# Kernel tuning notes

Hardware: AMD Instinct MI355X
Metric: run time of the kernel (lower is better)

Reference implementation:

```python
import jax, jax.numpy as jnp
import numpy as np

B, C_IN, C_OUT, K, H, W = 16, 256, 512, 7, 64, 64
PAD = K // 2


def setup_inputs() -> dict:
    key = jax.random.key(0)
    k1, k2, k3 = jax.random.split(key, 3)
    x = jax.random.normal(k1, (B, C_IN, H, W), dtype=jnp.float32)
    # depthwise weight: [out_channels=C_IN, in_channels//groups=1, k, k]
    fan_dw = 1 * K * K
    dw_w = jax.random.normal(k2, (C_IN, 1, K, K), dtype=jnp.float32) * np.sqrt(2.0 / fan_dw)
    dw_b = jnp.zeros((C_IN,), dtype=jnp.float32)
    # pointwise weight: [C_OUT, C_IN, 1, 1]
    pw_w = jax.random.normal(k3, (C_OUT, C_IN, 1, 1), dtype=jnp.float32) * np.sqrt(2.0 / C_IN)
    pw_b = jnp.zeros((C_OUT,), dtype=jnp.float32)
    return {"x": x, "dw_w": dw_w, "dw_b": dw_b, "pw_w": pw_w, "pw_b": pw_b}


def reference(x, dw_w, dw_b, pw_w, pw_b):
    # Depthwise conv (groups == C_in): cross-correlation, same as the torch
    # unfold+einsum construction with zero padding k//2.
    y = jax.lax.conv_general_dilated(
        x, dw_w,
        window_strides=(1, 1),
        padding=[(PAD, PAD), (PAD, PAD)],
        feature_group_count=C_IN,
        dimension_numbers=("NCHW", "OIHW", "NCHW"),
    )
    y = y + dw_b[None, :, None, None]
    # Pointwise 1x1 conv == per-pixel GEMM over channels.
    out = jnp.einsum("bchw,oc->bohw", y, pw_w[:, :, 0, 0])
    out = out + pw_b[None, :, None, None]
    return out
```

## Files before the change

kernel.cpp:

```cpp
#include <hip/hip_runtime.h>

typedef unsigned short US;
typedef __bf16 bf16x8 __attribute__((ext_vector_type(8)));
typedef float f32x4 __attribute__((ext_vector_type(4)));

__device__ __forceinline__ US f2bf(float f) {
  union { float f; unsigned u; } v; v.f = f;
  unsigned r = v.u + 0x7fffu + ((v.u >> 16) & 1u);
  return (US)(r >> 16);
}

__global__ __launch_bounds__(256) void k_convw(const float* __restrict__ pw,
                                               US* __restrict__ wb) {
  int i = (blockIdx.x * 256 + threadIdx.x) * 4;
  float4 v = *(const float4*)(pw + i);
  ushort4 s;
  s.x = f2bf(v.x); s.y = f2bf(v.y); s.z = f2bf(v.z); s.w = f2bf(v.w);
  *(ushort4*)(wb + i) = s;
}

__global__ __launch_bounds__(512, 4) void k_dw(const float* __restrict__ x,
                                               const float* __restrict__ dww,
                                               const float* __restrict__ dwb,
                                               US* __restrict__ y8) {
  const int bid = blockIdx.x;
  const int rg  = bid & 3;
  const int cg  = (bid >> 2) & 31;
  const int b   = bid >> 7;
  const int t   = threadIdx.x;
  const int w   = t >> 6;
  const int l   = t & 63;
  const int g   = l >> 4;
  const int cb  = l & 15;
  const int c   = __builtin_amdgcn_readfirstlane(cg * 8 + w);
  const float* xp = x + ((size_t)b * 256 + c) * 4096;
  float wv[49];
  const float* wp = dww + c * 49;
#pragma unroll
  for (int i = 0; i < 49; ++i) wv[i] = wp[i];
  const float bias = dwb[c];

  const int r0  = rg * 16;
  const int br  = r0 + g * 4;
  const int bcx = cb * 4;

  float acc[4][4];
#pragma unroll
  for (int o = 0; o < 4; ++o)
#pragma unroll
    for (int q = 0; q < 4; ++q) acc[o][q] = bias;

#pragma unroll
  for (int j = 0; j < 10; ++j) {
    const int r = br - 3 + j;
    float L[12];
    if ((unsigned)r < 64u) {
      const float* rp = xp + r * 64 + bcx;
      float4 a = (bcx >= 4) ? *(const float4*)(rp - 4) : float4{0.f, 0.f, 0.f, 0.f};
      float4 bb = *(const float4*)(rp);
      float4 cc = (bcx < 60) ? *(const float4*)(rp + 4) : float4{0.f, 0.f, 0.f, 0.f};
      L[0]=a.x; L[1]=a.y; L[2]=a.z;  L[3]=a.w;
      L[4]=bb.x; L[5]=bb.y; L[6]=bb.z; L[7]=bb.w;
      L[8]=cc.x; L[9]=cc.y; L[10]=cc.z; L[11]=cc.w;
    } else {
#pragma unroll
      for (int i2 = 0; i2 < 12; ++i2) L[i2] = 0.f;
    }
#pragma unroll
    for (int o = 0; o < 4; ++o) {
      if (j - o >= 0 && j - o <= 6) {
        const int kh = j - o;
#pragma unroll
        for (int kw = 0; kw < 7; ++kw) {
          const float wk = wv[kh * 7 + kw];
#pragma unroll
          for (int q = 0; q < 4; ++q)
            acc[o][q] = fmaf(L[q + kw + 1], wk, acc[o][q]);
        }
      }
    }
  }

  __shared__ US t8[8][1024];
#pragma unroll
  for (int o = 0; o < 4; ++o) {
    ushort4 s;
    s.x = f2bf(acc[o][0]); s.y = f2bf(acc[o][1]);
    s.z = f2bf(acc[o][2]); s.w = f2bf(acc[o][3]);
    *(ushort4*)&t8[w][(g * 4 + o) * 64 + bcx] = s;
  }
  __syncthreads();

  unsigned rc[8];
#pragma unroll
  for (int c2 = 0; c2 < 8; ++c2) rc[c2] = *(const unsigned*)&t8[c2][2 * t];
  uint4 A, B2;
  A.x  = __builtin_amdgcn_perm(rc[1], rc[0], 0x05040100u);
  A.y  = __builtin_amdgcn_perm(rc[3], rc[2], 0x05040100u);
  A.z  = __builtin_amdgcn_perm(rc[5], rc[4], 0x05040100u);
  A.w  = __builtin_amdgcn_perm(rc[7], rc[6], 0x05040100u);
  B2.x = __builtin_amdgcn_perm(rc[1], rc[0], 0x07060302u);
  B2.y = __builtin_amdgcn_perm(rc[3], rc[2], 0x07060302u);
  B2.z = __builtin_amdgcn_perm(rc[5], rc[4], 0x07060302u);
  B2.w = __builtin_amdgcn_perm(rc[7], rc[6], 0x07060302u);
  US* yb = y8 + (((size_t)b * 32 + cg) * 4096 + r0 * 64) * 8 + (size_t)t * 16;
  *(uint4*)(yb)     = A;
  *(uint4*)(yb + 8) = B2;
}

__global__ __launch_bounds__(256, 2) void k_pw(const US* __restrict__ y8,
                                               const US* __restrict__ wb,
                                               const float* __restrict__ pwb,
                                               float* __restrict__ out) {
  const int bid = blockIdx.x;
  const int s   = ((bid & 7) << 8) | (bid >> 3);
  const int b   = s >> 7;
  const int rr  = s & 127;
  const int nt  = rr >> 2;
  const int mt  = rr & 3;
  const int o0  = mt * 128;
  const int hw0 = nt * 128;

  __shared__ US lsA[2][128][72];
  __shared__ US lsB[2][128][72];
  const int tid  = threadIdx.x;
  const int lane = tid & 63;
  const int wid  = tid >> 6;
  const int wm   = wid >> 1, wn = wid & 1;
  const int strow = tid >> 3;
  const int scg   = tid & 7;
  const int bg    = tid >> 5;
  const int bl    = tid & 31;

  const f32x4 fzero = {0.f, 0.f, 0.f, 0.f};
  f32x4 acc[4][4];
#pragma unroll
  for (int m = 0; m < 4; ++m)
#pragma unroll
    for (int n = 0; n < 4; ++n) acc[m][n] = fzero;

  uint4 ra[4], rb[4];
#pragma unroll
  for (int i = 0; i < 4; ++i) {
    ra[i] = *(const uint4*)(wb + (size_t)(o0 + i * 32 + strow) * 256 + scg * 8);
    rb[i] = *(const uint4*)(y8 + ((size_t)(b * 32 + bg) * 4096 + hw0 + bl + 32 * i) * 8);
  }
#pragma unroll
  for (int i = 0; i < 4; ++i) {
    *(uint4*)&lsA[0][i * 32 + strow][scg * 8] = ra[i];
    *(uint4*)&lsB[0][bl + 32 * i][bg * 8]     = rb[i];
  }
  __syncthreads();

  for (int kt = 0; kt < 4; ++kt) {
    const int cur = kt & 1;
    if (kt < 3) {
      const int ck = (kt + 1) * 64;
#pragma unroll
      for (int i = 0; i < 4; ++i) {
        ra[i] = *(const uint4*)(wb + (size_t)(o0 + i * 32 + strow) * 256 + ck + scg * 8);
        rb[i] = *(const uint4*)(y8 + ((size_t)(b * 32 + (ck >> 3) + bg) * 4096 + hw0 + bl + 32 * i) * 8);
      }
    }
    bf16x8 af[2][4], bfr[2][4];
#pragma unroll
    for (int kk = 0; kk < 2; ++kk) {
      const int kcol = kk * 32 + (lane >> 4) * 8;
#pragma unroll
      for (int m = 0; m < 4; ++m)
        af[kk][m] = *reinterpret_cast<const bf16x8*>(&lsA[cur][wm * 64 + m * 16 + (lane & 15)][kcol]);
#pragma unroll
      for (int n = 0; n < 4; ++n)
        bfr[kk][n] = *reinterpret_cast<const bf16x8*>(&lsB[cur][wn * 64 + n * 16 + (lane & 15)][kcol]);
    }
#pragma unroll
    for (int kk = 0; kk < 2; ++kk)
#pragma unroll
      for (int m = 0; m < 4; ++m)
#pragma unroll
        for (int n = 0; n < 4; ++n)
          acc[m][n] = __builtin_amdgcn_mfma_f32_16x16x32_bf16(bfr[kk][n], af[kk][m], acc[m][n], 0, 0, 0);

    if (kt < 3) {
#pragma unroll
      for (int i = 0; i < 4; ++i) {
        *(uint4*)&lsA[cur ^ 1][i * 32 + strow][scg * 8] = ra[i];
        *(uint4*)&lsB[cur ^ 1][bl + 32 * i][bg * 8]     = rb[i];
      }
      __syncthreads();
    }
  }

#pragma unroll
  for (int m = 0; m < 4; ++m) {
    const int o  = o0 + wm * 64 + m * 16 + (lane & 15);
    const float bv = pwb[o];
    float* orow = out + (((size_t)b * 512 + o) * 4096) + hw0 + wn * 64 + (lane >> 4) * 4;
#pragma unroll
    for (int n = 0; n < 4; ++n) {
      f32x4 v = acc[m][n];
      v[0] += bv; v[1] += bv; v[2] += bv; v[3] += bv;
      *(f32x4*)(orow + n * 16) = v;
    }
  }
}

extern "C" void kernel_launch(void* const* d_in, const int* in_sizes, int n_in,
                              void* d_out, int out_size, void* d_ws, size_t ws_size,
                              hipStream_t stream) {
  const float* x   = (const float*)d_in[0];
  const float* dww = (const float*)d_in[1];
  const float* dwb = (const float*)d_in[2];
  const float* pww = (const float*)d_in[3];
  const float* pwb = (const float*)d_in[4];
  float* out = (float*)d_out;

  char* ws = (char*)d_ws;
  US* y8  = (US*)ws;
  US* wbf = (US*)(ws + 33554432);

  k_convw<<<128,  256, 0, stream>>>(pww, wbf);
  k_dw   <<<2048, 512, 0, stream>>>(x, dww, dwb, y8);
  k_pw   <<<2048, 256, 0, stream>>>(y8, wbf, pwb, out);
}
```

Measured before the change: 87.99 us.

## Process full image per depthwise block with rolling row window; nontemporal output stores

```diff
diff --git a/kernel.cpp b/kernel.cpp
--- a/kernel.cpp
+++ b/kernel.cpp
@@ -24,14 +24,13 @@
                                                const float* __restrict__ dwb,
                                                US* __restrict__ y8) {
   const int bid = blockIdx.x;
-  const int rg  = bid & 3;
-  const int cg  = (bid >> 2) & 31;
-  const int b   = bid >> 7;
+  const int cg  = bid & 31;
+  const int b   = bid >> 5;
   const int t   = threadIdx.x;
   const int w   = t >> 6;
   const int l   = t & 63;
-  const int g   = l >> 4;
-  const int cb  = l & 15;
+  const int s   = l & 15;
+  const int band = l >> 4;
   const int c   = __builtin_amdgcn_readfirstlane(cg * 8 + w);
   const float* xp = x + ((size_t)b * 256 + c) * 4096;
   float wv[49];
@@ -40,72 +39,76 @@
   for (int i = 0; i < 49; ++i) wv[i] = wp[i];
   const float bias = dwb[c];
 
-  const int r0  = rg * 16;
-  const int br  = r0 + g * 4;
-  const int bcx = cb * 4;
-
-  float acc[4][4];
-#pragma unroll
-  for (int o = 0; o < 4; ++o)
-#pragma unroll
-    for (int q = 0; q < 4; ++q) acc[o][q] = bias;
-
-#pragma unroll
-  for (int j = 0; j < 10; ++j) {
-    const int r = br - 3 + j;
-    float L[12];
-    if ((unsigned)r < 64u) {
-      const float* rp = xp + r * 64 + bcx;
-      float4 a = (bcx >= 4) ? *(const float4*)(rp - 4) : float4{0.f, 0.f, 0.f, 0.f};
-      float4 bb = *(const float4*)(rp);
-      float4 cc = (bcx < 60) ? *(const float4*)(rp + 4) : float4{0.f, 0.f, 0.f, 0.f};
-      L[0]=a.x; L[1]=a.y; L[2]=a.z;  L[3]=a.w;
-      L[4]=bb.x; L[5]=bb.y; L[6]=bb.z; L[7]=bb.w;
-      L[8]=cc.x; L[9]=cc.y; L[10]=cc.z; L[11]=cc.w;
-    } else {
-#pragma unroll
-      for (int i2 = 0; i2 < 12; ++i2) L[i2] = 0.f;
-    }
-#pragma unroll
-    for (int o = 0; o < 4; ++o) {
-      if (j - o >= 0 && j - o <= 6) {
-        const int kh = j - o;
-#pragma unroll
-        for (int kw = 0; kw < 7; ++kw) {
-          const float wk = wv[kh * 7 + kw];
-#pragma unroll
-          for (int q = 0; q < 4; ++q)
-            acc[o][q] = fmaf(L[q + kw + 1], wk, acc[o][q]);
-        }
+  const int bcx   = s * 4;
+  const int rbase = band * 16;
+
+  __shared__ US t8[8][4096];
+
+  float win[7][12];
+  const float4 fz = {0.f, 0.f, 0.f, 0.f};
+
+#define LOADROW(Ldst, r)                                                     \
+  do {                                                                       \
+    if ((unsigned)(r) < 64u) {                                               \
+      const float* rp = xp + (r) * 64 + bcx;                                 \
+      float4 a_ = (bcx >= 4) ? *(const float4*)(rp - 4) : fz;                \
+      float4 b_ = *(const float4*)(rp);                                      \
+      float4 c_ = (bcx < 60) ? *(const float4*)(rp + 4) : fz;                \
+      (Ldst)[0] = a_.x; (Ldst)[1] = a_.y; (Ldst)[2]  = a_.z; (Ldst)[3]  = a_.w; \
+      (Ldst)[4] = b_.x; (Ldst)[5] = b_.y; (Ldst)[6]  = b_.z; (Ldst)[7]  = b_.w; \
+      (Ldst)[8] = c_.x; (Ldst)[9] = c_.y; (Ldst)[10] = c_.z; (Ldst)[11] = c_.w; \
+    } else {                                                                 \
+      _Pragma("unroll")                                                      \
+      for (int z_ = 0; z_ < 12; ++z_) (Ldst)[z_] = 0.f;                      \
+    }                                                                        \
+  } while (0)
+
+#pragma unroll
+  for (int idx = 0; idx < 6; ++idx) LOADROW(win[idx], rbase - 3 + idx);
+
+#pragma unroll
+  for (int o = 0; o < 16; ++o) {
+    LOADROW(win[(o + 6) % 7], rbase + o + 3);
+    float a0 = bias, a1 = bias, a2 = bias, a3 = bias;
+#pragma unroll
+    for (int kh = 0; kh < 7; ++kh) {
+      const float* L = win[(o + kh) % 7];
+#pragma unroll
+      for (int kw = 0; kw < 7; ++kw) {
+        const float wk = wv[kh * 7 + kw];
+        a0 = fmaf(L[kw + 1], wk, a0);
+        a1 = fmaf(L[kw + 2], wk, a1);
+        a2 = fmaf(L[kw + 3], wk, a2);
+        a3 = fmaf(L[kw + 4], wk, a3);
       }
     }
-  }
-
-  __shared__ US t8[8][1024];
-#pragma unroll
-  for (int o = 0; o < 4; ++o) {
-    ushort4 s;
-    s.x = f2bf(acc[o][0]); s.y = f2bf(acc[o][1]);
-    s.z = f2bf(acc[o][2]); s.w = f2bf(acc[o][3]);
-    *(ushort4*)&t8[w][(g * 4 + o) * 64 + bcx] = s;
+    ushort4 sv;
+    sv.x = f2bf(a0); sv.y = f2bf(a1); sv.z = f2bf(a2); sv.w = f2bf(a3);
+    *(ushort4*)&t8[w][(rbase + o) * 64 + bcx] = sv;
   }
   __syncthreads();
 
-  unsigned rc[8];
-#pragma unroll
-  for (int c2 = 0; c2 < 8; ++c2) rc[c2] = *(const unsigned*)&t8[c2][2 * t];
-  uint4 A, B2;
-  A.x  = __builtin_amdgcn_perm(rc[1], rc[0], 0x05040100u);
-  A.y  = __builtin_amdgcn_perm(rc[3], rc[2], 0x05040100u);
-  A.z  = __builtin_amdgcn_perm(rc[5], rc[4], 0x05040100u);
-  A.w  = __builtin_amdgcn_perm(rc[7], rc[6], 0x05040100u);
-  B2.x = __builtin_amdgcn_perm(rc[1], rc[0], 0x07060302u);
-  B2.y = __builtin_amdgcn_perm(rc[3], rc[2], 0x07060302u);
-  B2.z = __builtin_amdgcn_perm(rc[5], rc[4], 0x07060302u);
-  B2.w = __builtin_amdgcn_perm(rc[7], rc[6], 0x07060302u);
-  US* yb = y8 + (((size_t)b * 32 + cg) * 4096 + r0 * 64) * 8 + (size_t)t * 16;
-  *(uint4*)(yb)     = A;
-  *(uint4*)(yb + 8) = B2;
+  const size_t ybase = ((size_t)b * 32 + cg) * 4096;
+#pragma unroll
+  for (int it = 0; it < 4; ++it) {
+    const int px = it * 1024 + t * 2;
+    unsigned rc[8];
+#pragma unroll
+    for (int c2 = 0; c2 < 8; ++c2) rc[c2] = *(const unsigned*)&t8[c2][px];
+    uint4 A, B2;
+    A.x  = __builtin_amdgcn_perm(rc[1], rc[0], 0x05040100u);
+    A.y  = __builtin_amdgcn_perm(rc[3], rc[2], 0x05040100u);
+    A.z  = __builtin_amdgcn_perm(rc[5], rc[4], 0x05040100u);
+    A.w  = __builtin_amdgcn_perm(rc[7], rc[6], 0x05040100u);
+    B2.x = __builtin_amdgcn_perm(rc[1], rc[0], 0x07060302u);
+    B2.y = __builtin_amdgcn_perm(rc[3], rc[2], 0x07060302u);
+    B2.z = __builtin_amdgcn_perm(rc[5], rc[4], 0x07060302u);
+    B2.w = __builtin_amdgcn_perm(rc[7], rc[6], 0x07060302u);
+    US* yb = y8 + (ybase + px) * 8;
+    *(uint4*)(yb)     = A;
+    *(uint4*)(yb + 8) = B2;
+  }
+#undef LOADROW
 }
 
 __global__ __launch_bounds__(256, 2) void k_pw(const US* __restrict__ y8,
@@ -200,7 +203,7 @@
     for (int n = 0; n < 4; ++n) {
       f32x4 v = acc[m][n];
       v[0] += bv; v[1] += bv; v[2] += bv; v[3] += bv;
-      *(f32x4*)(orow + n * 16) = v;
+      __builtin_nontemporal_store(v, (f32x4*)(orow + n * 16));
     }
   }
 }
@@ -219,7 +222,7 @@
   US* y8  = (US*)ws;
   US* wbf = (US*)(ws + 33554432);
 
-  k_convw<<<128,  256, 0, stream>>>(pww, wbf);
-  k_dw   <<<2048, 512, 0, stream>>>(x, dww, dwb, y8);
+  k_convw<<<128, 256, 0, stream>>>(pww, wbf);
+  k_dw   <<<512, 512, 0, stream>>>(x, dww, dwb, y8);
   k_pw   <<<2048, 256, 0, stream>>>(y8, wbf, pwb, out);
 }
```

Measured after the change: 169.4 us. +92.5%, slower.
